# Kernel tuning notes

Hardware: AMD Instinct MI355X
Metric: run time of the kernel (lower is better)

The kernel has to match this reference:

```python
import jax, jax.numpy as jnp
import numpy as np

# Fixed multi-scale geometry implied by the module's hard-coded reshapes
# (48^2=2304, 24^2=576, 12^2=144; Len_q = 576).
SPATIAL = [(48, 48), (24, 24), (12, 12)]
NH, NP, NL = 6, 4, 3  # num_heads, num_points, num_levels


def _process_reference_points(rp):
    """rp: (B, 3024, 2) normalized refs over 3 levels -> (B, 576, 2).
    Mirrors the part1/part2/part3 averaging in MSDeformAttn.forward."""
    B = rp.shape[0]
    p1 = rp[:, :2304].reshape(B, 48, 48, 2).mean(axis=(1, 2))[:, None, :]
    p1 = jnp.broadcast_to(p1, (B, 576, 2))
    p2 = rp[:, 2304:2880].reshape(B, 576, 2)
    p3 = rp[:, 2880:].reshape(B, 12, 12, 2)
    p3 = jax.image.resize(p3, (B, 24, 24, 2), 'bilinear')  # align_corners=False
    p3 = p3.reshape(B, 576, 2)
    return (p1 + p2 + p3) / 3.0


def _bilinear_sample(val_l, coords, Hl, Wl):
    """val_l: (B, Hl*Wl, nh, d) one level's values.
    coords: (B, Lq, nh, P, 2) normalized (x, y) sampling locations.
    Returns (B, Lq, P, nh, d) bilinearly sampled values (zero padding)."""
    B, Lq, nh, P, _ = coords.shape
    px = coords[..., 0] * Wl - 0.5
    py = coords[..., 1] * Hl - 0.5
    x0 = jnp.floor(px)
    y0 = jnp.floor(py)
    lx = px - x0
    ly = py - y0
    x0i = x0.astype(jnp.int32)
    y0i = y0.astype(jnp.int32)

    def _flat(a):  # (B,Lq,nh,P) -> (B,Lq*P,nh,1) matching value layout
        return a.transpose(0, 1, 3, 2).reshape(B, Lq * P, nh, 1)

    def gather(xi, yi):
        valid = (xi >= 0) & (xi < Wl) & (yi >= 0) & (yi < Hl)
        xi_c = jnp.clip(xi, 0, Wl - 1)
        yi_c = jnp.clip(yi, 0, Hl - 1)
        idx = _flat(yi_c * Wl + xi_c)
        v = jnp.take_along_axis(val_l, idx, axis=1)  # (B,Lq*P,nh,d)
        return v * _flat(valid).astype(val_l.dtype)

    w00 = _flat((1 - lx) * (1 - ly))
    w10 = _flat(lx * (1 - ly))
    w01 = _flat((1 - lx) * ly)
    w11 = _flat(lx * ly)
    out = (gather(x0i, y0i) * w00 + gather(x0i + 1, y0i) * w10 +
           gather(x0i, y0i + 1) * w01 + gather(x0i + 1, y0i + 1) * w11)
    return out.reshape(B, Lq, P, nh, -1)


def setup_inputs() -> dict:
    key = jax.random.key(0)
    ks = jax.random.split(key, 8)
    B, C = 32, 384
    Lq, Lv = 576, 3024
    # reference points exactly as get_reference_points builds them
    refs = []
    for (Hl, Wl) in SPATIAL:
        ry, rx = np.meshgrid(np.linspace(0.5, Hl - 0.5, Hl) / Hl,
                             np.linspace(0.5, Wl - 0.5, Wl) / Wl, indexing='ij')
        refs.append(np.stack([rx.ravel(), ry.ravel()], -1))
    rp = np.concatenate(refs, 0).astype(np.float32)  # (3024, 2)
    rp = np.broadcast_to(rp[None, :, None, :], (B, Lv, 1, 2)).copy()
    s = 1.0 / np.sqrt(C)
    return {
        'query': jax.random.normal(ks[0], (B, Lq, C), jnp.float32),
        'value': jax.random.normal(ks[1], (B, Lv, C), jnp.float32),
        'reference_points': jnp.asarray(rp),
        'W_value': jax.random.normal(ks[2], (C, C), jnp.float32) * s,
        'b_value': jnp.zeros((C,), jnp.float32),
        'W_off': jax.random.normal(ks[3], (C, NH * NL * NP * 2), jnp.float32) * 0.01,
        'b_off': jnp.zeros((NH * NL * NP * 2,), jnp.float32),
        'W_attn': jax.random.normal(ks[4], (C, NH * NL * NP), jnp.float32) * s,
        'b_attn': jnp.zeros((NH * NL * NP,), jnp.float32),
        'W_out': jax.random.normal(ks[5], (C, C), jnp.float32) * s,
        'b_out': jnp.zeros((C,), jnp.float32),
    }


def reference(query, value, reference_points, W_value, b_value, W_off, b_off,
              W_attn, b_attn, W_out, b_out):
    B, Lq, C = query.shape
    d = C // NH
    val = (value @ W_value + b_value).reshape(B, -1, NH, d)
    off = (query @ W_off + b_off).reshape(B, Lq, NH, NL, NP, 2)
    attn = jax.nn.softmax((query @ W_attn + b_attn)
                          .reshape(B, Lq, NH, NL * NP), axis=-1)
    attn = attn.reshape(B, Lq, NH, NL, NP)
    ref = _process_reference_points(reference_points.reshape(B, -1, 2))
    coords = off + ref[:, :, None, None, None, :]  # (B,Lq,nh,L,P,2)
    out = jnp.zeros((B, Lq, NH, d), query.dtype)
    start = 0
    for l, (Hl, Wl) in enumerate(SPATIAL):
        val_l = val[:, start:start + Hl * Wl]
        sampled = _bilinear_sample(val_l, coords[:, :, :, l], Hl, Wl)
        out = out + jnp.einsum('bqpnd,bqnp->bqnd', sampled, attn[:, :, :, l])
        start += Hl * Wl
    return out.reshape(B, Lq, NH * d) @ W_out + b_out
```

## Files before the change

kernel.cpp:

```cpp
#include <hip/hip_runtime.h>
#include <cmath>

#define B_SZ   32
#define LQ     576
#define LV     3024
#define CDIM   384
#define NHEAD  6
#define DHEAD  64
#define NLVL   3
#define NPTS   4
#define NPROJ  216

typedef short  bx4 __attribute__((ext_vector_type(4)));
typedef short  bx8 __attribute__((ext_vector_type(8)));
typedef float  fx4 __attribute__((ext_vector_type(4)));

__device__ __forceinline__ short f2bf(float f) {
    unsigned u = __builtin_bit_cast(unsigned, f);
    unsigned r = (u + 0x7FFFu + ((u >> 16) & 1u)) >> 16;
    return (short)r;
}
__device__ __forceinline__ float bf2f(unsigned short u) {
    return __builtin_bit_cast(float, ((unsigned)u) << 16);
}

__global__ __launch_bounds__(256) void cast_transpose_kernel(
    const float* __restrict__ W, short* __restrict__ Wt, int K, int N)
{
    int idx = blockIdx.x * 256 + threadIdx.x;
    if (idx >= K * N) return;
    int n = idx / K, k = idx - n * K;
    Wt[idx] = f2bf(W[(size_t)k * N + n]);
}

__global__ __launch_bounds__(256) void prep_proj_kernel(
    const float* __restrict__ W_off, const float* __restrict__ b_off,
    const float* __restrict__ W_attn, const float* __restrict__ b_attn,
    short* __restrict__ Wh, short* __restrict__ Wl, float* __restrict__ bc)
{
    int idx = blockIdx.x * 256 + threadIdx.x;
    if (idx >= NPROJ * CDIM) return;
    int n = idx / CDIM, k = idx - n * CDIM;
    float w = (n < 144) ? W_off[(size_t)k * 144 + n]
                        : W_attn[(size_t)k * 72 + (n - 144)];
    short h = f2bf(w);
    float hf = bf2f((unsigned short)h);
    Wh[idx] = h;
    Wl[idx] = f2bf(w - hf);
    if (idx < NPROJ) bc[idx] = (idx < 144) ? b_off[idx] : b_attn[idx - 144];
}

template <bool A_FP32, bool OUT_BF16>
__global__ __launch_bounds__(256, 2) void gemm_regB_kernel(
    const void* __restrict__ Av, const short* __restrict__ Wt,
    const float* __restrict__ bias, void* __restrict__ Cout,
    int M, int K)
{
    constexpr int N = 384;
    __shared__ short As[128 * 72];

    const int tid = threadIdx.x;
    const int m0 = (blockIdx.x >> 1) * 128;
    const int n0 = (blockIdx.x & 1) * 192;

    const int w  = tid >> 6;
    const int l  = tid & 63;
    const int wr = (w & 1) * 64;
    const int wc = (w >> 1) * 96;
    const int lr = l & 15;
    const int ko = (l >> 4) * 8;

    const short* Bp = Wt + (size_t)(n0 + wc + lr) * K + ko;

    fx4 acc[4][6] = {};

    for (int k0 = 0; k0 < K; k0 += 64) {
        bx8 bfr[2][6];
        #pragma unroll
        for (int ks = 0; ks < 2; ++ks)
            #pragma unroll
            for (int j = 0; j < 6; ++j)
                bfr[ks][j] = *(const bx8*)(Bp + (size_t)j * 16 * K + k0 + ks * 32);

        if (A_FP32) {
            const float* A = (const float*)Av;
            #pragma unroll
            for (int r = 0; r < 8; ++r) {
                const int id = tid + r * 256;
                const int m  = id >> 4;
                const int kq = (id & 15) << 2;
                const float4 v = *(const float4*)(A + (size_t)(m0 + m) * K + k0 + kq);
                bx4 s;
                s[0] = f2bf(v.x); s[1] = f2bf(v.y); s[2] = f2bf(v.z); s[3] = f2bf(v.w);
                *(bx4*)&As[m * 72 + kq] = s;
            }
        } else {
            const short* A = (const short*)Av;
            #pragma unroll
            for (int r = 0; r < 4; ++r) {
                const int id = tid + r * 256;
                const int m  = id >> 3;
                const int k8 = (id & 7) << 3;
                *(bx8*)&As[m * 72 + k8] = *(const bx8*)(A + (size_t)(m0 + m) * K + k0 + k8);
            }
        }
        __syncthreads();

        #pragma unroll
        for (int ks = 0; ks < 2; ++ks) {
            bx8 af[4];
            #pragma unroll
            for (int i = 0; i < 4; ++i)
                af[i] = *(const bx8*)&As[(wr + i * 16 + lr) * 72 + ks * 32 + ko];
            #pragma unroll
            for (int i = 0; i < 4; ++i)
                #pragma unroll
                for (int j = 0; j < 6; ++j)
                    acc[i][j] = __builtin_amdgcn_mfma_f32_16x16x32_bf16(
                        af[i], bfr[ks][j], acc[i][j], 0, 0, 0);
        }
        __syncthreads();
    }

    const int rrow = (l >> 4) * 4;
    #pragma unroll
    for (int j = 0; j < 6; ++j) {
        const int col = n0 + wc + j * 16 + lr;
        const float bv = bias[col];
        #pragma unroll
        for (int i = 0; i < 4; ++i) {
            const int row = m0 + wr + i * 16 + rrow;
            #pragma unroll
            for (int r = 0; r < 4; ++r) {
                if (OUT_BF16)
                    ((short*)Cout)[(size_t)(row + r) * N + col] = f2bf(acc[i][j][r] + bv);
                else
                    ((float*)Cout)[(size_t)(row + r) * N + col] = acc[i][j][r] + bv;
            }
        }
    }
}

__global__ __launch_bounds__(256) void gemm_proj_split_kernel(
    const float* __restrict__ A, const short* __restrict__ Wh,
    const short* __restrict__ Wl, const float* __restrict__ bias,
    float* __restrict__ C, int M, int N, int K)
{
    __shared__ short Ah[128 * 40];
    __shared__ short Al[128 * 40];
    __shared__ short Bh[128 * 40];
    __shared__ short Bl[128 * 40];

    const int tid = threadIdx.x;
    const int m0 = blockIdx.y * 128;
    const int n0 = blockIdx.x * 128;

    const int kq = (tid & 7) << 2;
    const int rw = tid >> 3;

    const int w  = tid >> 6;
    const int l  = tid & 63;
    const int mw = (w & 1) * 64;
    const int nw = (w >> 1) * 64;
    const int lr = l & 15;
    const int ko = (l >> 4) * 8;

    fx4 acc[4][4] = {};

    for (int k0 = 0; k0 < K; k0 += 32) {
        #pragma unroll
        for (int r = 0; r < 4; ++r) {
            const int m = rw + r * 32;
            const float4 v = *(const float4*)(A + (size_t)(m0 + m) * K + k0 + kq);
            bx4 sh, sl;
            #pragma unroll
            for (int t = 0; t < 4; ++t) {
                const float f = ((const float*)&v)[t];
                const short h = f2bf(f);
                sh[t] = h;
                sl[t] = f2bf(f - bf2f((unsigned short)h));
            }
            *(bx4*)&Ah[m * 40 + kq] = sh;
            *(bx4*)&Al[m * 40 + kq] = sl;

            bx4 wh = {}, wl = {};
            if (n0 + m < N) {
                wh = *(const bx4*)(Wh + (size_t)(n0 + m) * K + k0 + kq);
                wl = *(const bx4*)(Wl + (size_t)(n0 + m) * K + k0 + kq);
            }
            *(bx4*)&Bh[m * 40 + kq] = wh;
            *(bx4*)&Bl[m * 40 + kq] = wl;
        }
        __syncthreads();

        bx8 ah[4], al[4], bh[4], bl[4];
        #pragma unroll
        for (int i = 0; i < 4; ++i) {
            ah[i] = *(const bx8*)&Ah[(mw + i * 16 + lr) * 40 + ko];
            al[i] = *(const bx8*)&Al[(mw + i * 16 + lr) * 40 + ko];
        }
        #pragma unroll
        for (int j = 0; j < 4; ++j) {
            bh[j] = *(const bx8*)&Bh[(nw + j * 16 + lr) * 40 + ko];
            bl[j] = *(const bx8*)&Bl[(nw + j * 16 + lr) * 40 + ko];
        }
        #pragma unroll
        for (int i = 0; i < 4; ++i)
            #pragma unroll
            for (int j = 0; j < 4; ++j) {
                acc[i][j] = __builtin_amdgcn_mfma_f32_16x16x32_bf16(al[i], bh[j], acc[i][j], 0, 0, 0);
                acc[i][j] = __builtin_amdgcn_mfma_f32_16x16x32_bf16(ah[i], bl[j], acc[i][j], 0, 0, 0);
                acc[i][j] = __builtin_amdgcn_mfma_f32_16x16x32_bf16(ah[i], bh[j], acc[i][j], 0, 0, 0);
            }
        __syncthreads();
    }

    const int rrow = (l >> 4) * 4;
    #pragma unroll
    for (int j = 0; j < 4; ++j) {
        const int col = n0 + nw + j * 16 + lr;
        if (col >= N) continue;
        const float bv = bias[col];
        #pragma unroll
        for (int i = 0; i < 4; ++i) {
            const int row = m0 + mw + i * 16 + rrow;
            #pragma unroll
            for (int r = 0; r < 4; ++r)
                C[(size_t)(row + r) * N + col] = acc[i][j][r] + bv;
        }
    }
}

__global__ __launch_bounds__(256) void ref_kernel(
    const float* __restrict__ rp, float* __restrict__ refp)
{
    const int b = blockIdx.x;
    const float* r = rp + (size_t)b * LV * 2;
    const int tid = threadIdx.x;

    __shared__ float redx[256], redy[256];
    float sx = 0.f, sy = 0.f;
    for (int i = tid; i < 2304; i += 256) {
        sx += r[2 * i + 0];
        sy += r[2 * i + 1];
    }
    redx[tid] = sx; redy[tid] = sy;
    __syncthreads();
    for (int s = 128; s > 0; s >>= 1) {
        if (tid < s) { redx[tid] += redx[tid + s]; redy[tid] += redy[tid + s]; }
        __syncthreads();
    }
    const float p1x = redx[0] * (1.f / 2304.f);
    const float p1y = redy[0] * (1.f / 2304.f);

    const float* g = r + 2880 * 2;
    for (int q = tid; q < 576; q += 256) {
        const float p2x = r[(2304 + q) * 2 + 0];
        const float p2y = r[(2304 + q) * 2 + 1];
        const int qy = q / 24, qx = q % 24;
        const float syc = fminf(fmaxf(0.5f * qy - 0.25f, 0.f), 11.f);
        const float sxc = fminf(fmaxf(0.5f * qx - 0.25f, 0.f), 11.f);
        int y0 = min((int)syc, 10);
        int x0 = min((int)sxc, 10);
        const float fy = syc - (float)y0, fx = sxc - (float)x0;
        const float v00x = g[(y0 * 12 + x0) * 2 + 0],     v00y = g[(y0 * 12 + x0) * 2 + 1];
        const float v10x = g[(y0 * 12 + x0 + 1) * 2 + 0], v10y = g[(y0 * 12 + x0 + 1) * 2 + 1];
        const float v01x = g[((y0 + 1) * 12 + x0) * 2 + 0],     v01y = g[((y0 + 1) * 12 + x0) * 2 + 1];
        const float v11x = g[((y0 + 1) * 12 + x0 + 1) * 2 + 0], v11y = g[((y0 + 1) * 12 + x0 + 1) * 2 + 1];
        const float p3x = (1.f - fy) * ((1.f - fx) * v00x + fx * v10x)
                        + fy * ((1.f - fx) * v01x + fx * v11x);
        const float p3y = (1.f - fy) * ((1.f - fx) * v00y + fx * v10y)
                        + fy * ((1.f - fx) * v01y + fx * v11y);
        refp[((size_t)b * LQ + q) * 2 + 0] = (p1x + p2x + p3x) * (1.f / 3.f);
        refp[((size_t)b * LQ + q) * 2 + 1] = (p1y + p2y + p3y) * (1.f / 3.f);
    }
}

__global__ __launch_bounds__(384) void sample_kernel(
    const unsigned short* __restrict__ val, const float* __restrict__ proj,
    const float* __restrict__ refp, short* __restrict__ mid)
{
    const int i = blockIdx.x;
    const int g = i & 7;
    const int r = i >> 3;
    const int b = g * 4 + (r / LQ);
    const int q = r - (r / LQ) * LQ;
    const int bq = b * LQ + q;
    const int tid = threadIdx.x;

    __shared__ float attn[72];
    __shared__ int   sloc[72][4];
    __shared__ float swt[72][4];

    if (tid < 72) {
        attn[tid] = proj[(size_t)bq * NPROJ + 144 + tid];

        const int h = tid / 12;
        const int rr = tid % 12;
        const int l = rr >> 2;
        const int p = rr & 3;

        const int HL[3] = {48, 24, 12};
        const int ST[3] = {0, 2304, 2880};
        const int Hl = HL[l], Wl = HL[l], st = ST[l];

        const float rx = refp[bq * 2 + 0];
        const float ry = refp[bq * 2 + 1];
        const int oc = ((h * NLVL + l) * NPTS + p) * 2;
        const float cx = proj[(size_t)bq * NPROJ + oc + 0] + rx;
        const float cy = proj[(size_t)bq * NPROJ + oc + 1] + ry;

        const float px = cx * (float)Wl - 0.5f;
        const float py = cy * (float)Hl - 0.5f;
        const float x0f = floorf(px), y0f = floorf(py);
        const float lx = px - x0f, ly = py - y0f;
        const int x0 = (int)x0f, y0 = (int)y0f;

        #pragma unroll
        for (int k = 0; k < 4; ++k) {
            const int dx = k & 1, dy = k >> 1;
            const int xi = x0 + dx, yi = y0 + dy;
            const bool v = (xi >= 0) && (xi < Wl) && (yi >= 0) && (yi < Hl);
            const int xc = min(max(xi, 0), Wl - 1);
            const int yc = min(max(yi, 0), Hl - 1);
            sloc[tid][k] = st + yc * Wl + xc;
            const float wx = dx ? lx : 1.f - lx;
            const float wy = dy ? ly : 1.f - ly;
            swt[tid][k] = v ? wx * wy : 0.f;
        }
    }
    __syncthreads();

    if (tid < NHEAD) {
        float mx = -1e30f;
        #pragma unroll
        for (int j = 0; j < 12; ++j) mx = fmaxf(mx, attn[tid * 12 + j]);
        float s = 0.f;
        #pragma unroll
        for (int j = 0; j < 12; ++j) {
            const float e = expf(attn[tid * 12 + j] - mx);
            attn[tid * 12 + j] = e;
            s += e;
        }
        const float inv = 1.f / s;
        #pragma unroll
        for (int j = 0; j < 12; ++j) attn[tid * 12 + j] *= inv;
    }
    __syncthreads();

    const int h = tid >> 6;
    const int c = tid & 63;
    const unsigned short* vb = val + (size_t)b * LV * CDIM + h * DHEAD + c;
    float acc = 0.f;
    #pragma unroll
    for (int s = 0; s < 12; ++s) {
        const int j = h * 12 + s;
        const float a = attn[j];
        const float sum = swt[j][0] * bf2f(vb[(size_t)sloc[j][0] * CDIM])
                        + swt[j][1] * bf2f(vb[(size_t)sloc[j][1] * CDIM])
                        + swt[j][2] * bf2f(vb[(size_t)sloc[j][2] * CDIM])
                        + swt[j][3] * bf2f(vb[(size_t)sloc[j][3] * CDIM]);
        acc += a * sum;
    }
    mid[(size_t)bq * CDIM + tid] = f2bf(acc);
}

extern "C" void kernel_launch(void* const* d_in, const int* in_sizes, int n_in,
                              void* d_out, int out_size, void* d_ws, size_t ws_size,
                              hipStream_t stream)
{
    (void)in_sizes; (void)n_in; (void)out_size; (void)ws_size;

    const float* query   = (const float*)d_in[0];
    const float* value   = (const float*)d_in[1];
    const float* rp      = (const float*)d_in[2];
    const float* W_value = (const float*)d_in[3];
    const float* b_value = (const float*)d_in[4];
    const float* W_off   = (const float*)d_in[5];
    const float* b_off   = (const float*)d_in[6];
    const float* W_attn  = (const float*)d_in[7];
    const float* b_attn  = (const float*)d_in[8];
    const float* W_out   = (const float*)d_in[9];
    const float* b_out   = (const float*)d_in[10];
    float* out = (float*)d_out;

    char* p = (char*)d_ws;
    auto take = [&](size_t bytes) { char* q = p; p += (bytes + 255) & ~(size_t)255; return q; };
    short* val  = (short*)take((size_t)B_SZ * LV * CDIM * 2);
    short* mid  = (short*)take((size_t)B_SZ * LQ * CDIM * 2);
    short* Wtv  = (short*)take((size_t)CDIM * CDIM * 2);
    short* Wto  = (short*)take((size_t)CDIM * CDIM * 2);
    short* Wh   = (short*)take((size_t)NPROJ * CDIM * 2);
    short* Wl   = (short*)take((size_t)NPROJ * CDIM * 2);
    float* proj = (float*)take((size_t)B_SZ * LQ * NPROJ * 4);
    float* refp = (float*)take((size_t)B_SZ * LQ * 2 * 4);
    float* bc   = (float*)take((size_t)NPROJ * 4);

    const int Mv = B_SZ * LV;
    const int Mq = B_SZ * LQ;

    cast_transpose_kernel<<<(CDIM * CDIM + 255) / 256, 256, 0, stream>>>(
        W_value, Wtv, CDIM, CDIM);
    cast_transpose_kernel<<<(CDIM * CDIM + 255) / 256, 256, 0, stream>>>(
        W_out, Wto, CDIM, CDIM);
    prep_proj_kernel<<<(NPROJ * CDIM + 255) / 256, 256, 0, stream>>>(
        W_off, b_off, W_attn, b_attn, Wh, Wl, bc);

    gemm_regB_kernel<true, true><<<(Mv / 128) * 2, 256, 0, stream>>>(
        value, Wtv, b_value, val, Mv, CDIM);
    gemm_proj_split_kernel<<<dim3((NPROJ + 127) / 128, Mq / 128), 256, 0, stream>>>(
        query, Wh, Wl, bc, proj, Mq, NPROJ, CDIM);
    ref_kernel<<<B_SZ, 256, 0, stream>>>(rp, refp);
    sample_kernel<<<Mq, 384, 0, stream>>>(
        (const unsigned short*)val, proj, refp, mid);
    gemm_regB_kernel<false, false><<<(Mq / 128) * 2, 256, 0, stream>>>(
        mid, Wto, b_out, out, Mq, CDIM);
}
```

Baseline: 456.2 us.

## Use single fp16 MFMA for projection, unify GEMMs, vectorize sampling

The query projection's split-bf16 GEMM, which issued three MFMAs per tile, is replaced by one fp16 MFMA pass over a weight matrix padded to 256 columns. All three GEMMs now go through one 128x128-tile kernel that stages B in LDS and allows 3 blocks per CU, instead of holding B fragments in registers. The sampling kernel now runs 192 threads, each handling two channels with 32-bit loads and a packed store. The goal is fewer MFMA instructions and better memory efficiency. The cost is lower accuracy in the sampling offsets (fp16 instead of an emulated near-fp32 split) and a changed GEMM tile shape.

Result: faster. 426.8 us (-6.5%).

```diff
diff --git a/kernel.cpp b/kernel.cpp
--- a/kernel.cpp
+++ b/kernel.cpp
@@ -10,10 +10,12 @@
 #define NLVL   3
 #define NPTS   4
 #define NPROJ  216
-
-typedef short  bx4 __attribute__((ext_vector_type(4)));
-typedef short  bx8 __attribute__((ext_vector_type(8)));
-typedef float  fx4 __attribute__((ext_vector_type(4)));
+#define NPROJP 256
+
+typedef short    bx4 __attribute__((ext_vector_type(4)));
+typedef short    bx8 __attribute__((ext_vector_type(8)));
+typedef float    fx4 __attribute__((ext_vector_type(4)));
+typedef _Float16 hx8 __attribute__((ext_vector_type(8)));
 
 __device__ __forceinline__ short f2bf(float f) {
     unsigned u = __builtin_bit_cast(unsigned, f);
@@ -23,6 +25,9 @@
 __device__ __forceinline__ float bf2f(unsigned short u) {
     return __builtin_bit_cast(float, ((unsigned)u) << 16);
 }
+__device__ __forceinline__ short f2h(float f) {
+    return __builtin_bit_cast(short, (_Float16)f);
+}
 
 __global__ __launch_bounds__(256) void cast_transpose_kernel(
     const float* __restrict__ W, short* __restrict__ Wt, int K, int N)
@@ -33,56 +38,56 @@
     Wt[idx] = f2bf(W[(size_t)k * N + n]);
 }
 
-__global__ __launch_bounds__(256) void prep_proj_kernel(
+__global__ __launch_bounds__(256) void prep_proj_f16_kernel(
     const float* __restrict__ W_off, const float* __restrict__ b_off,
     const float* __restrict__ W_attn, const float* __restrict__ b_attn,
-    short* __restrict__ Wh, short* __restrict__ Wl, float* __restrict__ bc)
+    short* __restrict__ Wf, float* __restrict__ bc)
 {
     int idx = blockIdx.x * 256 + threadIdx.x;
-    if (idx >= NPROJ * CDIM) return;
+    if (idx >= NPROJP * CDIM) return;
     int n = idx / CDIM, k = idx - n * CDIM;
-    float w = (n < 144) ? W_off[(size_t)k * 144 + n]
-                        : W_attn[(size_t)k * 72 + (n - 144)];
-    short h = f2bf(w);
-    float hf = bf2f((unsigned short)h);
-    Wh[idx] = h;
-    Wl[idx] = f2bf(w - hf);
-    if (idx < NPROJ) bc[idx] = (idx < 144) ? b_off[idx] : b_attn[idx - 144];
-}
-
-template <bool A_FP32, bool OUT_BF16>
-__global__ __launch_bounds__(256, 2) void gemm_regB_kernel(
-    const void* __restrict__ Av, const short* __restrict__ Wt,
+    float w = 0.f;
+    if (n < 144)           w = W_off[(size_t)k * 144 + n];
+    else if (n < NPROJ)    w = W_attn[(size_t)k * 72 + (n - 144)];
+    Wf[idx] = f2h(w);
+    if (idx < NPROJP)
+        bc[idx] = (idx < 144) ? b_off[idx]
+                 : (idx < NPROJ ? b_attn[idx - 144] : 0.f);
+}
+
+template <int ATYPE, bool F16, bool OUT_BF16, bool NGUARD>
+__global__ __launch_bounds__(256, 3) void gemm128_kernel(
+    const void* __restrict__ Av, const short* __restrict__ Bt,
     const float* __restrict__ bias, void* __restrict__ Cout,
-    int M, int K)
-{
-    constexpr int N = 384;
+    int M, int K, int Nact, int ldc)
+{
     __shared__ short As[128 * 72];
+    __shared__ short Bs[128 * 72];
 
     const int tid = threadIdx.x;
-    const int m0 = (blockIdx.x >> 1) * 128;
-    const int n0 = (blockIdx.x & 1) * 192;
+    const int n0 = blockIdx.x * 128;
+    const int m0 = blockIdx.y * 128;
 
     const int w  = tid >> 6;
     const int l  = tid & 63;
     const int wr = (w & 1) * 64;
-    const int wc = (w >> 1) * 96;
+    const int wc = (w >> 1) * 64;
     const int lr = l & 15;
     const int ko = (l >> 4) * 8;
 
-    const short* Bp = Wt + (size_t)(n0 + wc + lr) * K + ko;
-
-    fx4 acc[4][6] = {};
+    fx4 acc[4][4] = {};
 
     for (int k0 = 0; k0 < K; k0 += 64) {
-        bx8 bfr[2][6];
-        #pragma unroll
-        for (int ks = 0; ks < 2; ++ks)
-            #pragma unroll
-            for (int j = 0; j < 6; ++j)
-                bfr[ks][j] = *(const bx8*)(Bp + (size_t)j * 16 * K + k0 + ks * 32);
-
-        if (A_FP32) {
+        if (ATYPE == 1) {
+            const short* A = (const short*)Av;
+            #pragma unroll
+            for (int r = 0; r < 4; ++r) {
+                const int id = tid + r * 256;
+                const int m  = id >> 3;
+                const int k8 = (id & 7) << 3;
+                *(bx8*)&As[m * 72 + k8] = *(const bx8*)(A + (size_t)(m0 + m) * K + k0 + k8);
+            }
+        } else {
             const float* A = (const float*)Av;
             #pragma unroll
             for (int r = 0; r < 8; ++r) {
@@ -91,142 +96,64 @@
                 const int kq = (id & 15) << 2;
                 const float4 v = *(const float4*)(A + (size_t)(m0 + m) * K + k0 + kq);
                 bx4 s;
-                s[0] = f2bf(v.x); s[1] = f2bf(v.y); s[2] = f2bf(v.z); s[3] = f2bf(v.w);
+                if (ATYPE == 0) {
+                    s[0] = f2bf(v.x); s[1] = f2bf(v.y); s[2] = f2bf(v.z); s[3] = f2bf(v.w);
+                } else {
+                    s[0] = f2h(v.x);  s[1] = f2h(v.y);  s[2] = f2h(v.z);  s[3] = f2h(v.w);
+                }
                 *(bx4*)&As[m * 72 + kq] = s;
             }
-        } else {
-            const short* A = (const short*)Av;
-            #pragma unroll
-            for (int r = 0; r < 4; ++r) {
-                const int id = tid + r * 256;
-                const int m  = id >> 3;
-                const int k8 = (id & 7) << 3;
-                *(bx8*)&As[m * 72 + k8] = *(const bx8*)(A + (size_t)(m0 + m) * K + k0 + k8);
-            }
+        }
+        #pragma unroll
+        for (int r = 0; r < 4; ++r) {
+            const int id = tid + r * 256;
+            const int n  = id >> 3;
+            const int k8 = (id & 7) << 3;
+            *(bx8*)&Bs[n * 72 + k8] = *(const bx8*)(Bt + (size_t)(n0 + n) * K + k0 + k8);
         }
         __syncthreads();
 
         #pragma unroll
         for (int ks = 0; ks < 2; ++ks) {
-            bx8 af[4];
+            bx8 af[4], bf[4];
             #pragma unroll
             for (int i = 0; i < 4; ++i)
                 af[i] = *(const bx8*)&As[(wr + i * 16 + lr) * 72 + ks * 32 + ko];
             #pragma unroll
+            for (int j = 0; j < 4; ++j)
+                bf[j] = *(const bx8*)&Bs[(wc + j * 16 + lr) * 72 + ks * 32 + ko];
+            #pragma unroll
             for (int i = 0; i < 4; ++i)
                 #pragma unroll
-                for (int j = 0; j < 6; ++j)
-                    acc[i][j] = __builtin_amdgcn_mfma_f32_16x16x32_bf16(
-                        af[i], bfr[ks][j], acc[i][j], 0, 0, 0);
-        }
-        __syncthreads();
-    }
-
-    const int rrow = (l >> 4) * 4;
-    #pragma unroll
-    for (int j = 0; j < 6; ++j) {
-        const int col = n0 + wc + j * 16 + lr;
-        const float bv = bias[col];
-        #pragma unroll
-        for (int i = 0; i < 4; ++i) {
-            const int row = m0 + wr + i * 16 + rrow;
-            #pragma unroll
-            for (int r = 0; r < 4; ++r) {
-                if (OUT_BF16)
-                    ((short*)Cout)[(size_t)(row + r) * N + col] = f2bf(acc[i][j][r] + bv);
-                else
-                    ((float*)Cout)[(size_t)(row + r) * N + col] = acc[i][j][r] + bv;
-            }
-        }
-    }
-}
-
-__global__ __launch_bounds__(256) void gemm_proj_split_kernel(
-    const float* __restrict__ A, const short* __restrict__ Wh,
-    const short* __restrict__ Wl, const float* __restrict__ bias,
-    float* __restrict__ C, int M, int N, int K)
-{
-    __shared__ short Ah[128 * 40];
-    __shared__ short Al[128 * 40];
-    __shared__ short Bh[128 * 40];
-    __shared__ short Bl[128 * 40];
-
-    const int tid = threadIdx.x;
-    const int m0 = blockIdx.y * 128;
-    const int n0 = blockIdx.x * 128;
-
-    const int kq = (tid & 7) << 2;
-    const int rw = tid >> 3;
-
-    const int w  = tid >> 6;
-    const int l  = tid & 63;
-    const int mw = (w & 1) * 64;
-    const int nw = (w >> 1) * 64;
-    const int lr = l & 15;
-    const int ko = (l >> 4) * 8;
-
-    fx4 acc[4][4] = {};
-
-    for (int k0 = 0; k0 < K; k0 += 32) {
-        #pragma unroll
-        for (int r = 0; r < 4; ++r) {
-            const int m = rw + r * 32;
-            const float4 v = *(const float4*)(A + (size_t)(m0 + m) * K + k0 + kq);
-            bx4 sh, sl;
-            #pragma unroll
-            for (int t = 0; t < 4; ++t) {
-                const float f = ((const float*)&v)[t];
-                const short h = f2bf(f);
-                sh[t] = h;
-                sl[t] = f2bf(f - bf2f((unsigned short)h));
-            }
-            *(bx4*)&Ah[m * 40 + kq] = sh;
-            *(bx4*)&Al[m * 40 + kq] = sl;
-
-            bx4 wh = {}, wl = {};
-            if (n0 + m < N) {
-                wh = *(const bx4*)(Wh + (size_t)(n0 + m) * K + k0 + kq);
-                wl = *(const bx4*)(Wl + (size_t)(n0 + m) * K + k0 + kq);
-            }
-            *(bx4*)&Bh[m * 40 + kq] = wh;
-            *(bx4*)&Bl[m * 40 + kq] = wl;
-        }
-        __syncthreads();
-
-        bx8 ah[4], al[4], bh[4], bl[4];
-        #pragma unroll
-        for (int i = 0; i < 4; ++i) {
-            ah[i] = *(const bx8*)&Ah[(mw + i * 16 + lr) * 40 + ko];
-            al[i] = *(const bx8*)&Al[(mw + i * 16 + lr) * 40 + ko];
-        }
-        #pragma unroll
-        for (int j = 0; j < 4; ++j) {
-            bh[j] = *(const bx8*)&Bh[(nw + j * 16 + lr) * 40 + ko];
-            bl[j] = *(const bx8*)&Bl[(nw + j * 16 + lr) * 40 + ko];
-        }
-        #pragma unroll
-        for (int i = 0; i < 4; ++i)
-            #pragma unroll
-            for (int j = 0; j < 4; ++j) {
-                acc[i][j] = __builtin_amdgcn_mfma_f32_16x16x32_bf16(al[i], bh[j], acc[i][j], 0, 0, 0);
-                acc[i][j] = __builtin_amdgcn_mfma_f32_16x16x32_bf16(ah[i], bl[j], acc[i][j], 0, 0, 0);
-                acc[i][j] = __builtin_amdgcn_mfma_f32_16x16x32_bf16(ah[i], bh[j], acc[i][j], 0, 0, 0);
-            }
+                for (int j = 0; j < 4; ++j) {
+                    if (F16)
+                        acc[i][j] = __builtin_amdgcn_mfma_f32_16x16x32_f16(
+                            __builtin_bit_cast(hx8, af[i]),
+                            __builtin_bit_cast(hx8, bf[j]), acc[i][j], 0, 0, 0);
+                    else
+                        acc[i][j] = __builtin_amdgcn_mfma_f32_16x16x32_bf16(
+                            af[i], bf[j], acc[i][j], 0, 0, 0);
+                }
+        }
         __syncthreads();
     }
 
     const int rrow = (l >> 4) * 4;
     #pragma unroll
     for (int j = 0; j < 4; ++j) {
-        const int col = n0 + nw + j * 16 + lr;
-        if (col >= N) continue;
+        const int col = n0 + wc + j * 16 + lr;
+        if (NGUARD && col >= Nact) continue;
         const float bv = bias[col];
         #pragma unroll
         for (int i = 0; i < 4; ++i) {
-            const int row = m0 + mw + i * 16 + rrow;
-            #pragma unroll
-            for (int r = 0; r < 4; ++r)
-                C[(size_t)(row + r) * N + col] = acc[i][j][r] + bv;
+            const int row = m0 + wr + i * 16 + rrow;
+            #pragma unroll
+            for (int r = 0; r < 4; ++r) {
+                if (OUT_BF16)
+                    ((short*)Cout)[(size_t)(row + r) * ldc + col] = f2bf(acc[i][j][r] + bv);
+                else
+                    ((float*)Cout)[(size_t)(row + r) * ldc + col] = acc[i][j][r] + bv;
+            }
         }
     }
 }
@@ -276,9 +203,9 @@
     }
 }
 
-__global__ __launch_bounds__(384) void sample_kernel(
+__global__ __launch_bounds__(192) void sample_kernel(
     const unsigned short* __restrict__ val, const float* __restrict__ proj,
-    const float* __restrict__ refp, short* __restrict__ mid)
+    const float* __restrict__ refp, unsigned* __restrict__ mid)
 {
     const int i = blockIdx.x;
     const int g = i & 7;
@@ -348,21 +275,29 @@
     }
     __syncthreads();
 
-    const int h = tid >> 6;
-    const int c = tid & 63;
-    const unsigned short* vb = val + (size_t)b * LV * CDIM + h * DHEAD + c;
-    float acc = 0.f;
+    const int h  = tid >> 5;
+    const int c2 = (tid & 31) << 1;
+    const unsigned* vp = (const unsigned*)(val + (size_t)b * LV * CDIM + h * DHEAD + c2);
+    float acc0 = 0.f, acc1 = 0.f;
     #pragma unroll
     for (int s = 0; s < 12; ++s) {
         const int j = h * 12 + s;
         const float a = attn[j];
-        const float sum = swt[j][0] * bf2f(vb[(size_t)sloc[j][0] * CDIM])
-                        + swt[j][1] * bf2f(vb[(size_t)sloc[j][1] * CDIM])
-                        + swt[j][2] * bf2f(vb[(size_t)sloc[j][2] * CDIM])
-                        + swt[j][3] * bf2f(vb[(size_t)sloc[j][3] * CDIM]);
-        acc += a * sum;
-    }
-    mid[(size_t)bq * CDIM + tid] = f2bf(acc);
+        float s0 = 0.f, s1 = 0.f;
+        #pragma unroll
+        for (int k = 0; k < 4; ++k) {
+            const unsigned u = vp[(size_t)sloc[j][k] * (CDIM / 2)];
+            const float lo = __builtin_bit_cast(float, u << 16);
+            const float hi = __builtin_bit_cast(float, u & 0xFFFF0000u);
+            s0 += swt[j][k] * lo;
+            s1 += swt[j][k] * hi;
+        }
+        acc0 += a * s0;
+        acc1 += a * s1;
+    }
+    const unsigned lo = (unsigned)(unsigned short)f2bf(acc0);
+    const unsigned hi = (unsigned)(unsigned short)f2bf(acc1);
+    mid[((size_t)bq * CDIM + h * DHEAD + c2) >> 1] = lo | (hi << 16);
 }
 
 extern "C" void kernel_launch(void* const* d_in, const int* in_sizes, int n_in,
@@ -390,11 +325,10 @@
     short* mid  = (short*)take((size_t)B_SZ * LQ * CDIM * 2);
     short* Wtv  = (short*)take((size_t)CDIM * CDIM * 2);
     short* Wto  = (short*)take((size_t)CDIM * CDIM * 2);
-    short* Wh   = (short*)take((size_t)NPROJ * CDIM * 2);
-    short* Wl   = (short*)take((size_t)NPROJ * CDIM * 2);
+    short* Wf   = (short*)take((size_t)NPROJP * CDIM * 2);
     float* proj = (float*)take((size_t)B_SZ * LQ * NPROJ * 4);
     float* refp = (float*)take((size_t)B_SZ * LQ * 2 * 4);
-    float* bc   = (float*)take((size_t)NPROJ * 4);
+    float* bc   = (float*)take((size_t)NPROJP * 4);
 
     const int Mv = B_SZ * LV;
     const int Mq = B_SZ * LQ;
@@ -403,16 +337,16 @@
         W_value, Wtv, CDIM, CDIM);
     cast_transpose_kernel<<<(CDIM * CDIM + 255) / 256, 256, 0, stream>>>(
         W_out, Wto, CDIM, CDIM);
-    prep_proj_kernel<<<(NPROJ * CDIM + 255) / 256, 256, 0, stream>>>(
-        W_off, b_off, W_attn, b_attn, Wh, Wl, bc);
-
-    gemm_regB_kernel<true, true><<<(Mv / 128) * 2, 256, 0, stream>>>(
-        value, Wtv, b_value, val, Mv, CDIM);
-    gemm_proj_split_kernel<<<dim3((NPROJ + 127) / 128, Mq / 128), 256, 0, stream>>>(
-        query, Wh, Wl, bc, proj, Mq, NPROJ, CDIM);
+    prep_proj_f16_kernel<<<(NPROJP * CDIM + 255) / 256, 256, 0, stream>>>(
+        W_off, b_off, W_attn, b_attn, Wf, bc);
+
+    gemm128_kernel<0, false, true, false><<<dim3(3, Mv / 128), 256, 0, stream>>>(
+        value, Wtv, b_value, val, Mv, CDIM, CDIM, CDIM);
+    gemm128_kernel<2, true, false, true><<<dim3(2, Mq / 128), 256, 0, stream>>>(
+        query, Wf, bc, proj, Mq, CDIM, NPROJ, NPROJ);
     ref_kernel<<<B_SZ, 256, 0, stream>>>(rp, refp);
-    sample_kernel<<<Mq, 384, 0, stream>>>(
-        (const unsigned short*)val, proj, refp, mid);
-    gemm_regB_kernel<false, false><<<(Mq / 128) * 2, 256, 0, stream>>>(
-        mid, Wto, b_out, out, Mq, CDIM);
-}
+    sample_kernel<<<Mq, 192, 0, stream>>>(
+        (const unsigned short*)val, proj, refp, (unsigned*)mid);
+    gemm128_kernel<1, false, false, false><<<dim3(3, Mq / 128), 256, 0, stream>>>(
+        mid, Wto, b_out, out, Mq, CDIM, CDIM, CDIM);
+}
```
